# Kernel optimization log

Hardware: AMD Instinct MI355X
Metric: run time of the kernel (lower is better)

Reference implementation:

```python
import jax, jax.numpy as jnp
import numpy as np

OUT_F, IN_F, N = 8192, 8192, 16

def setup_inputs() -> dict:
    key = jax.random.key(0)
    k1, k2 = jax.random.split(key)
    x = jax.random.normal(k1, (IN_F, N), dtype=jnp.float32)
    # symmetric int8 weights stored as int8 (quantized per-tensor)
    int8_weights = jax.random.randint(k2, (OUT_F, IN_F), -128, 128, dtype=jnp.int8)
    # power-of-two per-tensor scale, as produced by derive_int8_quant_parameters
    scaler = jnp.float32(2.0 ** -7)
    return {"x": x, "int8_weights": int8_weights, "scaler": scaler}

def reference(x, int8_weights, scaler):
    # dequant_weight: cast int8 -> fp32, multiply by per-tensor scaler
    fp_weights = int8_weights.astype(jnp.float32) * scaler  # [out, in]
    # forward: activation = W @ x  (weight on the left, x is [in, N])
    activation = jnp.matmul(fp_weights, x)  # [out, N]
    return activation
```

## Files before the change

### kernel.cpp

```cpp
#include <hip/hip_runtime.h>

typedef _Float16 half8 __attribute__((ext_vector_type(8)));
typedef float floatx4 __attribute__((ext_vector_type(4)));

constexpr int IN_F  = 8192;
constexpr int OUT_F = 8192;
constexpr int NCOL  = 16;

constexpr int WVS     = 8;
constexpr int KCHUNK  = IN_F / WVS;
constexpr int SUBK    = 128;
constexpr int NSUB    = KCHUNK / SUBK;
constexpr int STEPS   = SUBK / 32;
constexpr int NBLOCKS = OUT_F / 16;

__global__ __launch_bounds__(512, 4)
void lq_mfma_kernel(const float* __restrict__ x,
                    const void* __restrict__ wraw,
                    const float* __restrict__ scaler,
                    float* __restrict__ out)
{
    __shared__ float red[WVS * 256];

    const int tid  = threadIdx.x;
    const int lane = tid & 63;
    const int wv   = tid >> 6;
    const int m    = lane & 15;
    const int quad = lane >> 4;
    const int row0 = blockIdx.x * 16;
    const int k0   = wv * KCHUNK;

    const int* wi = (const int*)wraw;
    bool w_is_i32 = true;
    #pragma unroll
    for (int i = 0; i < 16; ++i) {
        int v = wi[i];
        w_is_i32 = w_is_i32 && (v >= -128) && (v <= 127);
    }

    const float* xp = x + (size_t)(k0 + quad * 8) * NCOL + m;
    floatx4 acc = {0.f, 0.f, 0.f, 0.f};

    if (w_is_i32) {
        const int* wrow = (const int*)wraw + (size_t)(row0 + m) * IN_F + k0 + quad * 8;
        #pragma unroll 1
        for (int sc = 0; sc < NSUB; ++sc) {
            const int kb = sc * SUBK;
            half8 bf[STEPS];
            #pragma unroll
            for (int st = 0; st < STEPS; ++st) {
                #pragma unroll
                for (int j = 0; j < 8; ++j)
                    bf[st][j] = (_Float16)xp[(kb + st * 32 + j) * NCOL];
            }
            #pragma unroll
            for (int st = 0; st < STEPS; ++st) {
                half8 af;
                #pragma unroll
                for (int j = 0; j < 8; ++j)
                    af[j] = (_Float16)wrow[kb + st * 32 + j];
                acc = __builtin_amdgcn_mfma_f32_16x16x32_f16(af, bf[st], acc, 0, 0, 0);
            }
        }
    } else {
        const signed char* wrow = (const signed char*)wraw + (size_t)(row0 + m) * IN_F + k0 + quad * 8;
        #pragma unroll 1
        for (int sc = 0; sc < NSUB; ++sc) {
            const int kb = sc * SUBK;
            half8 bf[STEPS];
            #pragma unroll
            for (int st = 0; st < STEPS; ++st) {
                #pragma unroll
                for (int j = 0; j < 8; ++j)
                    bf[st][j] = (_Float16)xp[(kb + st * 32 + j) * NCOL];
            }
            #pragma unroll
            for (int st = 0; st < STEPS; ++st) {
                const uint2 u = *(const uint2*)(wrow + kb + st * 32);
                half8 af;
                #pragma unroll
                for (int j = 0; j < 4; ++j) {
                    af[j]     = (_Float16)(int)(signed char)(u.x >> (8 * j));
                    af[j + 4] = (_Float16)(int)(signed char)(u.y >> (8 * j));
                }
                acc = __builtin_amdgcn_mfma_f32_16x16x32_f16(af, bf[st], acc, 0, 0, 0);
            }
        }
    }

    #pragma unroll
    for (int g = 0; g < 4; ++g)
        red[wv * 256 + (quad * 4 + g) * 16 + m] = acc[g];
    __syncthreads();

    if (tid < 256) {
        float sum = 0.f;
        #pragma unroll
        for (int v = 0; v < WVS; ++v)
            sum += red[v * 256 + tid];
        out[(size_t)(row0 + (tid >> 4)) * NCOL + (tid & 15)] = sum * scaler[0];
    }
}

extern "C" void kernel_launch(void* const* d_in, const int* in_sizes, int n_in,
                              void* d_out, int out_size, void* d_ws, size_t ws_size,
                              hipStream_t stream)
{
    const float* x      = (const float*)d_in[0];
    const void*  w      = d_in[1];
    const float* scaler = (const float*)d_in[2];
    float*       out    = (float*)d_out;

    lq_mfma_kernel<<<NBLOCKS, 512, 0, stream>>>(x, w, scaler, out);
}
```

Before: 379.6 us.

## Pre-transpose x to fp16 and double-buffer weight/x loads across windows

Adds a small pre-kernel that converts x to fp16 and transposes it into the workspace so each lane can load a half8 with one vector load instead of eight strided fp32 loads. The main kernel is restructured to prefetch the next window's weights (as uint4 vectors for the int32 path) and x fragments while the MFMAs for the current window run, and the loop is now fully unrolled. This is meant to hide global memory latency and reduce load instruction count. In exchange it adds a second launch, more register pressure from the double buffers, and depends on a workspace of adequate size.

```diff
diff --git a/kernel.cpp b/kernel.cpp
--- a/kernel.cpp
+++ b/kernel.cpp
@@ -7,15 +7,30 @@
 constexpr int OUT_F = 8192;
 constexpr int NCOL  = 16;
 
-constexpr int WVS     = 8;
-constexpr int KCHUNK  = IN_F / WVS;
-constexpr int SUBK    = 128;
-constexpr int NSUB    = KCHUNK / SUBK;
-constexpr int STEPS   = SUBK / 32;
+constexpr int WVS    = 8;
+constexpr int KCHUNK = IN_F / WVS;
+constexpr int WIN    = 128;
+constexpr int NWIN   = KCHUNK / WIN;
+constexpr int STEPS  = WIN / 32;
 constexpr int NBLOCKS = OUT_F / 16;
 
+__global__ __launch_bounds__(256)
+void xt_kernel(const float* __restrict__ x, _Float16* __restrict__ xt)
+{
+    const int t  = blockIdx.x * 256 + threadIdx.x;
+    const int n  = t >> 10;
+    const int kb = (t & 1023) * 8;
+    half8 v;
+    #pragma unroll
+    for (int j = 0; j < 8; ++j)
+        v[j] = (_Float16)x[(size_t)(kb + j) * NCOL + n];
+    *(half8*)(xt + (size_t)n * IN_F + kb) = v;
+}
+
+template<bool XT>
 __global__ __launch_bounds__(512, 4)
 void lq_mfma_kernel(const float* __restrict__ x,
+                    const _Float16* __restrict__ xt,
                     const void* __restrict__ wraw,
                     const float* __restrict__ scaler,
                     float* __restrict__ out)
@@ -38,53 +53,97 @@
         w_is_i32 = w_is_i32 && (v >= -128) && (v <= 127);
     }
 
-    const float* xp = x + (size_t)(k0 + quad * 8) * NCOL + m;
     floatx4 acc = {0.f, 0.f, 0.f, 0.f};
 
+    const _Float16* xtp = xt + (size_t)m * IN_F + k0 + quad * 8;
+    const float*    xp  = x + (size_t)(k0 + quad * 8) * NCOL + m;
+    auto load_bf = [&](int kb, half8* bf) {
+        if constexpr (XT) {
+            #pragma unroll
+            for (int st = 0; st < STEPS; ++st)
+                bf[st] = *(const half8*)(xtp + kb + st * 32);
+        } else {
+            #pragma unroll
+            for (int st = 0; st < STEPS; ++st)
+                #pragma unroll
+                for (int j = 0; j < 8; ++j)
+                    bf[st][j] = (_Float16)xp[(size_t)(kb + st * 32 + j) * NCOL];
+        }
+    };
+
     if (w_is_i32) {
-        const int* wrow = (const int*)wraw + (size_t)(row0 + m) * IN_F + k0 + quad * 8;
-        #pragma unroll 1
-        for (int sc = 0; sc < NSUB; ++sc) {
-            const int kb = sc * SUBK;
-            half8 bf[STEPS];
+        const uint4* wbase = (const uint4*)((const int*)wraw
+                             + (size_t)(row0 + m) * IN_F + k0 + quad * 8);
+        uint4 wa[2 * STEPS];
+        half8 af[STEPS];
+        half8 ba[2][STEPS];
+
+        #pragma unroll
+        for (int st = 0; st < STEPS; ++st) {
+            wa[st * 2]     = wbase[st * 8];
+            wa[st * 2 + 1] = wbase[st * 8 + 1];
+        }
+        load_bf(0, ba[0]);
+
+        #pragma unroll
+        for (int w = 0; w < NWIN; ++w) {
+            const int cur = w & 1, nxt = cur ^ 1;
+            half8 afc[STEPS];
             #pragma unroll
             for (int st = 0; st < STEPS; ++st) {
+                const uint4 a = wa[st * 2], b = wa[st * 2 + 1];
+                afc[st][0] = (_Float16)(int)a.x;  afc[st][1] = (_Float16)(int)a.y;
+                afc[st][2] = (_Float16)(int)a.z;  afc[st][3] = (_Float16)(int)a.w;
+                afc[st][4] = (_Float16)(int)b.x;  afc[st][5] = (_Float16)(int)b.y;
+                afc[st][6] = (_Float16)(int)b.z;  afc[st][7] = (_Float16)(int)b.w;
+            }
+            if (w + 1 < NWIN) {
+                const uint4* wn = wbase + (size_t)(w + 1) * (WIN / 4);
                 #pragma unroll
-                for (int j = 0; j < 8; ++j)
-                    bf[st][j] = (_Float16)xp[(kb + st * 32 + j) * NCOL];
+                for (int st = 0; st < STEPS; ++st) {
+                    wa[st * 2]     = wn[st * 8];
+                    wa[st * 2 + 1] = wn[st * 8 + 1];
+                }
+                load_bf((w + 1) * WIN, ba[nxt]);
             }
             #pragma unroll
-            for (int st = 0; st < STEPS; ++st) {
-                half8 af;
-                #pragma unroll
-                for (int j = 0; j < 8; ++j)
-                    af[j] = (_Float16)wrow[kb + st * 32 + j];
-                acc = __builtin_amdgcn_mfma_f32_16x16x32_f16(af, bf[st], acc, 0, 0, 0);
-            }
+            for (int st = 0; st < STEPS; ++st)
+                acc = __builtin_amdgcn_mfma_f32_16x16x32_f16(afc[st], ba[cur][st], acc, 0, 0, 0);
         }
     } else {
-        const signed char* wrow = (const signed char*)wraw + (size_t)(row0 + m) * IN_F + k0 + quad * 8;
-        #pragma unroll 1
-        for (int sc = 0; sc < NSUB; ++sc) {
-            const int kb = sc * SUBK;
-            half8 bf[STEPS];
+        const signed char* wbase = (const signed char*)wraw
+                                   + (size_t)(row0 + m) * IN_F + k0 + quad * 8;
+        uint2 wa[STEPS];
+        half8 ba[2][STEPS];
+
+        #pragma unroll
+        for (int st = 0; st < STEPS; ++st)
+            wa[st] = *(const uint2*)(wbase + st * 32);
+        load_bf(0, ba[0]);
+
+        #pragma unroll
+        for (int w = 0; w < NWIN; ++w) {
+            const int cur = w & 1, nxt = cur ^ 1;
+            half8 afc[STEPS];
             #pragma unroll
             for (int st = 0; st < STEPS; ++st) {
+                const uint2 u = wa[st];
                 #pragma unroll
-                for (int j = 0; j < 8; ++j)
-                    bf[st][j] = (_Float16)xp[(kb + st * 32 + j) * NCOL];
+                for (int j = 0; j < 4; ++j) {
+                    afc[st][j]     = (_Float16)(int)(signed char)(u.x >> (8 * j));
+                    afc[st][j + 4] = (_Float16)(int)(signed char)(u.y >> (8 * j));
+                }
+            }
+            if (w + 1 < NWIN) {
+                const signed char* wn = wbase + (size_t)(w + 1) * WIN;
+                #pragma unroll
+                for (int st = 0; st < STEPS; ++st)
+                    wa[st] = *(const uint2*)(wn + st * 32);
+                load_bf((w + 1) * WIN, ba[nxt]);
             }
             #pragma unroll
-            for (int st = 0; st < STEPS; ++st) {
-                const uint2 u = *(const uint2*)(wrow + kb + st * 32);
-                half8 af;
-                #pragma unroll
-                for (int j = 0; j < 4; ++j) {
-                    af[j]     = (_Float16)(int)(signed char)(u.x >> (8 * j));
-                    af[j + 4] = (_Float16)(int)(signed char)(u.y >> (8 * j));
-                }
-                acc = __builtin_amdgcn_mfma_f32_16x16x32_f16(af, bf[st], acc, 0, 0, 0);
-            }
+            for (int st = 0; st < STEPS; ++st)
+                acc = __builtin_amdgcn_mfma_f32_16x16x32_f16(afc[st], ba[cur][st], acc, 0, 0, 0);
         }
     }
 
@@ -98,7 +157,7 @@
         #pragma unroll
         for (int v = 0; v < WVS; ++v)
             sum += red[v * 256 + tid];
-        out[(size_t)(row0 + (tid >> 4)) * NCOL + (tid & 15)] = sum * scaler[0];
+        out[(size_t)row0 * NCOL + tid] = sum * scaler[0];
     }
 }
 
@@ -111,5 +170,12 @@
     const float* scaler = (const float*)d_in[2];
     float*       out    = (float*)d_out;
 
-    lq_mfma_kernel<<<NBLOCKS, 512, 0, stream>>>(x, w, scaler, out);
+    const size_t xt_bytes = (size_t)IN_F * NCOL * sizeof(_Float16);
+    if (ws_size >= xt_bytes) {
+        _Float16* xt = (_Float16*)d_ws;
+        xt_kernel<<<(IN_F * NCOL / 8) / 256, 256, 0, stream>>>(x, xt);
+        lq_mfma_kernel<true><<<NBLOCKS, 512, 0, stream>>>(x, xt, w, scaler, out);
+    } else {
+        lq_mfma_kernel<false><<<NBLOCKS, 512, 0, stream>>>(x, nullptr, w, scaler, out);
+    }
 }
```

Measured after the change: 389.6 us. 2.6% more time.

## Pre-transpose x to fp16 and double-buffer tiles into LDS via global_load_lds

Applied to the files above, without the earlier changes.

Adds a pre-pass kernel that converts x into a transposed fp16 buffer in workspace. The main kernel then streams swizzled 256-wide K tiles of weights and x directly into LDS with global_load_lds, double-buffering so each tile's load overlaps the previous tile's MFMA. All 8 waves share each tile, each covering a different k-slice, which replaces per-lane strided scalar global loads with coalesced 16-byte transfers. The cost is an extra kernel launch, two barriers per tile, and a dependence on workspace size, with the old path kept as a fallback.

```diff
diff --git a/kernel.cpp b/kernel.cpp
--- a/kernel.cpp
+++ b/kernel.cpp
@@ -2,25 +2,39 @@
 
 typedef _Float16 half8 __attribute__((ext_vector_type(8)));
 typedef float floatx4 __attribute__((ext_vector_type(4)));
+typedef int int4v __attribute__((ext_vector_type(4)));
 
 constexpr int IN_F  = 8192;
 constexpr int OUT_F = 8192;
 constexpr int NCOL  = 16;
 
 constexpr int WVS     = 8;
-constexpr int KCHUNK  = IN_F / WVS;
-constexpr int SUBK    = 128;
-constexpr int NSUB    = KCHUNK / SUBK;
-constexpr int STEPS   = SUBK / 32;
+constexpr int BK      = 256;
+constexpr int NT      = IN_F / BK;
 constexpr int NBLOCKS = OUT_F / 16;
 
+__global__ __launch_bounds__(256)
+void xt_kernel(const float* __restrict__ x, _Float16* __restrict__ xt)
+{
+    const int t  = blockIdx.x * 256 + threadIdx.x;
+    const int n  = t >> 10;
+    const int kb = (t & 1023) * 8;
+    half8 v;
+    #pragma unroll
+    for (int j = 0; j < 8; ++j)
+        v[j] = (_Float16)x[(size_t)(kb + j) * NCOL + n];
+    *(half8*)(xt + (size_t)n * IN_F + kb) = v;
+}
+
+template<bool XT>
 __global__ __launch_bounds__(512, 4)
 void lq_mfma_kernel(const float* __restrict__ x,
+                    const _Float16* __restrict__ xt,
                     const void* __restrict__ wraw,
                     const float* __restrict__ scaler,
                     float* __restrict__ out)
 {
-    __shared__ float red[WVS * 256];
+    __shared__ int smem[12288];
 
     const int tid  = threadIdx.x;
     const int lane = tid & 63;
@@ -28,7 +42,6 @@
     const int m    = lane & 15;
     const int quad = lane >> 4;
     const int row0 = blockIdx.x * 16;
-    const int k0   = wv * KCHUNK;
 
     const int* wi = (const int*)wraw;
     bool w_is_i32 = true;
@@ -38,56 +51,100 @@
         w_is_i32 = w_is_i32 && (v >= -128) && (v <= 127);
     }
 
-    const float* xp = x + (size_t)(k0 + quad * 8) * NCOL + m;
     floatx4 acc = {0.f, 0.f, 0.f, 0.f};
 
-    if (w_is_i32) {
-        const int* wrow = (const int*)wraw + (size_t)(row0 + m) * IN_F + k0 + quad * 8;
+    if (XT && w_is_i32) {
+        const int r0s = wv * 2, r1s = wv * 2 + 1;
+        const char* wsrc0 = (const char*)wraw + (size_t)(row0 + r0s) * (IN_F * 4)
+                          + ((lane * 16) ^ ((r0s & 7) << 4));
+        const char* wsrc1 = (const char*)wraw + (size_t)(row0 + r1s) * (IN_F * 4)
+                          + ((lane * 16) ^ ((r1s & 7) << 4));
+        const int   nst   = wv * 2 + (lane >> 5);
+        const char* xsrc  = (const char*)xt + (size_t)nst * (IN_F * 2)
+                          + (((lane & 31) * 16) ^ ((wv & 7) << 4));
+
+        const int aoff0 = m * 1024 + (((wv * 128) + quad * 32)      ^ ((m & 7) << 4));
+        const int aoff1 = m * 1024 + (((wv * 128) + quad * 32 + 16) ^ ((m & 7) << 4));
+        const int boff  = (m >> 1) * 1024 + (m & 1) * 512
+                        + (((wv * 64) + quad * 16) ^ (((m >> 1) & 7) << 4));
+
+        auto stage = [&](int t, int b) {
+            int* wd0 = smem + b * 4096 + r0s * 256;
+            int* wd1 = smem + b * 4096 + r1s * 256;
+            int* xd  = smem + 8192 + b * 2048 + wv * 256;
+            __builtin_amdgcn_global_load_lds(
+                (const __attribute__((address_space(1))) unsigned*)(wsrc0 + (size_t)t * 1024),
+                (__attribute__((address_space(3))) unsigned*)wd0, 16, 0, 0);
+            __builtin_amdgcn_global_load_lds(
+                (const __attribute__((address_space(1))) unsigned*)(wsrc1 + (size_t)t * 1024),
+                (__attribute__((address_space(3))) unsigned*)wd1, 16, 0, 0);
+            __builtin_amdgcn_global_load_lds(
+                (const __attribute__((address_space(1))) unsigned*)(xsrc + (size_t)t * 512),
+                (__attribute__((address_space(3))) unsigned*)xd, 16, 0, 0);
+        };
+
+        stage(0, 0);
         #pragma unroll 1
-        for (int sc = 0; sc < NSUB; ++sc) {
-            const int kb = sc * SUBK;
-            half8 bf[STEPS];
-            #pragma unroll
-            for (int st = 0; st < STEPS; ++st) {
+        for (int t = 0; t < NT; ++t) {
+            const int b = t & 1;
+            if (t + 1 < NT) {
+                stage(t + 1, b ^ 1);
+                asm volatile("s_waitcnt vmcnt(3)" ::: "memory");
+            } else {
+                asm volatile("s_waitcnt vmcnt(0)" ::: "memory");
+            }
+            __syncthreads();
+
+            const char* wb = (const char*)smem + b * 16384;
+            const char* xb = (const char*)smem + 32768 + b * 8192;
+            const int4v a0 = *(const int4v*)(wb + aoff0);
+            const int4v a1 = *(const int4v*)(wb + aoff1);
+            const half8 bf = *(const half8*)(xb + boff);
+            half8 af;
+            af[0] = (_Float16)a0[0];  af[1] = (_Float16)a0[1];
+            af[2] = (_Float16)a0[2];  af[3] = (_Float16)a0[3];
+            af[4] = (_Float16)a1[0];  af[5] = (_Float16)a1[1];
+            af[6] = (_Float16)a1[2];  af[7] = (_Float16)a1[3];
+            acc = __builtin_amdgcn_mfma_f32_16x16x32_f16(af, bf, acc, 0, 0, 0);
+
+            __syncthreads();
+        }
+    } else {
+        const int k0 = wv * 1024;
+        const float* xp = x + (size_t)(k0 + quad * 8) * NCOL + m;
+        if (w_is_i32) {
+            const int* wrow = (const int*)wraw + (size_t)(row0 + m) * IN_F + k0 + quad * 8;
+            #pragma unroll 1
+            for (int st = 0; st < 32; ++st) {
+                half8 bfr, afr;
+                #pragma unroll
+                for (int j = 0; j < 8; ++j) {
+                    bfr[j] = (_Float16)xp[(size_t)(st * 32 + j) * NCOL];
+                    afr[j] = (_Float16)wrow[st * 32 + j];
+                }
+                acc = __builtin_amdgcn_mfma_f32_16x16x32_f16(afr, bfr, acc, 0, 0, 0);
+            }
+        } else {
+            const signed char* wrow = (const signed char*)wraw + (size_t)(row0 + m) * IN_F + k0 + quad * 8;
+            #pragma unroll 1
+            for (int st = 0; st < 32; ++st) {
+                half8 bfr, afr;
                 #pragma unroll
                 for (int j = 0; j < 8; ++j)
-                    bf[st][j] = (_Float16)xp[(kb + st * 32 + j) * NCOL];
-            }
-            #pragma unroll
-            for (int st = 0; st < STEPS; ++st) {
-                half8 af;
+                    bfr[j] = (_Float16)xp[(size_t)(st * 32 + j) * NCOL];
+                const uint2 u = *(const uint2*)(wrow + st * 32);
                 #pragma unroll
-                for (int j = 0; j < 8; ++j)
-                    af[j] = (_Float16)wrow[kb + st * 32 + j];
-                acc = __builtin_amdgcn_mfma_f32_16x16x32_f16(af, bf[st], acc, 0, 0, 0);
+                for (int j = 0; j < 4; ++j) {
+                    afr[j]     = (_Float16)(int)(signed char)(u.x >> (8 * j));
+                    afr[j + 4] = (_Float16)(int)(signed char)(u.y >> (8 * j));
+                }
+                acc = __builtin_amdgcn_mfma_f32_16x16x32_f16(afr, bfr, acc, 0, 0, 0);
             }
         }
-    } else {
-        const signed char* wrow = (const signed char*)wraw + (size_t)(row0 + m) * IN_F + k0 + quad * 8;
-        #pragma unroll 1
-        for (int sc = 0; sc < NSUB; ++sc) {
-            const int kb = sc * SUBK;
-            half8 bf[STEPS];
-            #pragma unroll
-            for (int st = 0; st < STEPS; ++st) {
-                #pragma unroll
-                for (int j = 0; j < 8; ++j)
-                    bf[st][j] = (_Float16)xp[(kb + st * 32 + j) * NCOL];
-            }
-            #pragma unroll
-            for (int st = 0; st < STEPS; ++st) {
-                const uint2 u = *(const uint2*)(wrow + kb + st * 32);
-                half8 af;
-                #pragma unroll
-                for (int j = 0; j < 4; ++j) {
-                    af[j]     = (_Float16)(int)(signed char)(u.x >> (8 * j));
-                    af[j + 4] = (_Float16)(int)(signed char)(u.y >> (8 * j));
-                }
-                acc = __builtin_amdgcn_mfma_f32_16x16x32_f16(af, bf[st], acc, 0, 0, 0);
-            }
-        }
+        __syncthreads();
     }
 
+    float* red = (float*)smem;
     #pragma unroll
     for (int g = 0; g < 4; ++g)
         red[wv * 256 + (quad * 4 + g) * 16 + m] = acc[g];
@@ -98,7 +155,7 @@
         #pragma unroll
         for (int v = 0; v < WVS; ++v)
             sum += red[v * 256 + tid];
-        out[(size_t)(row0 + (tid >> 4)) * NCOL + (tid & 15)] = sum * scaler[0];
+        out[(size_t)row0 * NCOL + tid] = sum * scaler[0];
     }
 }
 
@@ -111,5 +168,12 @@
     const float* scaler = (const float*)d_in[2];
     float*       out    = (float*)d_out;
 
-    lq_mfma_kernel<<<NBLOCKS, 512, 0, stream>>>(x, w, scaler, out);
+    const size_t xt_bytes = (size_t)IN_F * NCOL * sizeof(_Float16);
+    if (ws_size >= xt_bytes) {
+        _Float16* xtp = (_Float16*)d_ws;
+        xt_kernel<<<(IN_F * NCOL / 8) / 256, 256, 0, stream>>>(x, xtp);
+        lq_mfma_kernel<true><<<NBLOCKS, 512, 0, stream>>>(x, xtp, w, scaler, out);
+    } else {
+        lq_mfma_kernel<false><<<NBLOCKS, 512, 0, stream>>>(x, nullptr, w, scaler, out);
+    }
 }
```

Result: faster. 366.0 us (-3.6%).
